# Optimization experiments

Hardware: AMD Instinct MI355X
Metric: run time of the kernel (lower is better)

## Reference

```python
import jax, jax.numpy as jnp
import numpy as np

B, N, E = 32, 196, 512      # batch, image regions, encoder_dim
D, EMB, V = 512, 512, 32000  # decoder_dim, embedding_dim, vocab
MAXLEN = 65


def setup_inputs() -> dict:
    key = jax.random.key(0)
    ks = jax.random.split(key, 16)
    s = lambda *sh: 1.0 / np.sqrt(sh[-1])
    return {
        "image_features": jax.random.normal(ks[0], (B, N, E), jnp.float32),
        "captions": jax.random.randint(ks[1], (B, MAXLEN), 0, V),
        "emb": jax.random.normal(ks[2], (V, EMB), jnp.float32) * 0.02,
        "Wh0": jax.random.normal(ks[3], (D, E), jnp.float32) * s(E),
        "bh0": jnp.zeros((D,), jnp.float32),
        "Wc0": jax.random.normal(ks[4], (D, E), jnp.float32) * s(E),
        "bc0": jnp.zeros((D,), jnp.float32),
        "Wenc": jax.random.normal(ks[5], (D, E), jnp.float32) * s(E),
        "Wdec": jax.random.normal(ks[6], (D, D), jnp.float32) * s(D),
        "v_att": jax.random.normal(ks[7], (D,), jnp.float32) * s(D),
        "W_ih": jax.random.normal(ks[8], (4 * D, EMB + E), jnp.float32) * s(EMB + E),
        "b_ih": jnp.zeros((4 * D,), jnp.float32),
        "W_hh": jax.random.normal(ks[9], (4 * D, D), jnp.float32) * s(D),
        "b_hh": jnp.zeros((4 * D,), jnp.float32),
        "Wfc": jax.random.normal(ks[10], (V, D), jnp.float32) * s(D),
        "bfc": jnp.zeros((V,), jnp.float32),
    }


def reference(image_features, captions, emb, Wh0, bh0, Wc0, bc0,
              Wenc, Wdec, v_att, W_ih, b_ih, W_hh, b_hh, Wfc, bfc):
    seq_len = captions.shape[1] - 1
    emb_caps = emb[captions]                     # [B, maxlen, EMB]
    xs = jnp.swapaxes(emb_caps[:, :seq_len], 0, 1)  # [T, B, EMB]

    feat_mean = image_features.mean(axis=1)      # [B, E]
    h0 = feat_mean @ Wh0.T + bh0                 # [B, D]
    c0 = feat_mean @ Wc0.T + bc0
    feat_proj = jnp.einsum('bne,de->bnd', image_features, Wenc)  # [B, N, D]

    def step(carry, xt):
        h, c = carry
        # Bahdanau additive attention over the N image regions
        e = jnp.einsum('bnd,d->bn', jnp.tanh(feat_proj + (h @ Wdec.T)[:, None, :]), v_att)
        alpha = jax.nn.softmax(e, axis=-1)                       # [B, N]
        ctx = jnp.einsum('bn,bne->be', alpha, image_features)    # [B, E]
        x = jnp.concatenate([xt, ctx], axis=-1)                  # [B, EMB+E]
        gates = x @ W_ih.T + b_ih + h @ W_hh.T + b_hh            # [B, 4D]
        i, f, g, o = jnp.split(gates, 4, axis=-1)
        c_new = jax.nn.sigmoid(f) * c + jax.nn.sigmoid(i) * jnp.tanh(g)
        h_new = jax.nn.sigmoid(o) * jnp.tanh(c_new)
        out = h_new @ Wfc.T + bfc                                # [B, V]
        return (h_new, c_new), (out, alpha)
    # dropout_p=0.0 -> dropout is identity (eval-mode reference)
    _, (outs, alphas) = jax.lax.scan(step, (h0, c0), xs)
    outputs = jnp.swapaxes(outs, 0, 1)            # [B, T, V]
    attention_weights = jnp.swapaxes(alphas, 0, 1)  # [B, T, N]
    return outputs, attention_weights
```

## Files before the change

kernel.cpp:

```cpp
#include <hip/hip_runtime.h>
#include <cstdint>
#include <cstddef>

typedef _Float16 half2_t __attribute__((ext_vector_type(2)));
typedef _Float16 half4_t __attribute__((ext_vector_type(4)));
typedef _Float16 half8_t __attribute__((ext_vector_type(8)));
typedef float    float4_t __attribute__((ext_vector_type(4)));

#define CAPLEN 65
#define PTLD 200
#define BARSTRIDE 32

#define AT_LD(p)     __hip_atomic_load((p), __ATOMIC_RELAXED, __HIP_MEMORY_SCOPE_AGENT)
#define AT_ST(p, v)  __hip_atomic_store((p), (v), __ATOMIC_RELAXED, __HIP_MEMORY_SCOPE_AGENT)

#if defined(__has_builtin)
#if __has_builtin(__builtin_amdgcn_fdot2)
#define HAS_FDOT2 1
#endif
#endif

__device__ __forceinline__ float fdot2f(half2_t a, half2_t b, float c) {
#ifdef HAS_FDOT2
  return __builtin_amdgcn_fdot2(a, b, c, false);
#else
  return c + (float)a[0]*(float)b[0] + (float)a[1]*(float)b[1];
#endif
}

__device__ __forceinline__ float fast_tanh(float x) {
  float e = __expf(2.f*x);
  return 1.f - 2.f/(e + 1.f);
}
__device__ __forceinline__ float fast_sig(float x) {
  return 1.f/(1.f + __expf(-x));
}

__global__ void cvt_k(const float* __restrict__ s, _Float16* __restrict__ d, int n) {
  int i = (blockIdx.x*blockDim.x + threadIdx.x)*4;
  if (i < n) {
    float4 v = *(const float4*)(s + i);
    half4_t h;
    h[0] = (_Float16)v.x; h[1] = (_Float16)v.y; h[2] = (_Float16)v.z; h[3] = (_Float16)v.w;
    *(half4_t*)(d + i) = h;
  }
}

__global__ void bias_sum_k(const float* __restrict__ a, const float* __restrict__ b,
                           float* __restrict__ o, unsigned* __restrict__ bar) {
  int i = blockIdx.x*blockDim.x + threadIdx.x;
  if (i < 2048) o[i] = a[i] + b[i];
  for (int j = i; j < 32*8*BARSTRIDE; j += 2048) bar[j] = 0u;
}

__global__ void gather_emb_k(const float* __restrict__ emb, const int* __restrict__ cap,
                             _Float16* __restrict__ X) {
  int r = blockIdx.x;
  int t = r >> 5, b = r & 31;
  int tok = cap[b*CAPLEN + t];
  const float* s = emb + (size_t)tok*512;
  _Float16* d = X + (size_t)r*512;
  for (int k = threadIdx.x; k < 512; k += blockDim.x) d[k] = (_Float16)s[k];
}

__global__ void init_state_k(const float* __restrict__ imgf,
                             const float* __restrict__ Wh0, const float* __restrict__ bh0,
                             const float* __restrict__ Wc0, const float* __restrict__ bc0,
                             float* __restrict__ c_state, unsigned* __restrict__ hpub2) {
  __shared__ float fm[512];
  __shared__ float hsh[512];
  int b = blockIdx.x, tid = threadIdx.x;
  for (int dI = tid; dI < 512; dI += 256) {
    float s = 0.f;
    const float* p = imgf + ((size_t)b*196)*512 + dI;
    for (int n = 0; n < 196; n++) s += p[(size_t)n*512];
    fm[dI] = s * (1.f/196.f);
  }
  __syncthreads();
  for (int dI = tid; dI < 512; dI += 256) {
    const float* wh = Wh0 + (size_t)dI*512;
    const float* wc = Wc0 + (size_t)dI*512;
    float h = bh0[dI], c = bc0[dI];
    for (int k = 0; k < 512; k++) { h += fm[k]*wh[k]; c += fm[k]*wc[k]; }
    hsh[dI] = h;
    c_state[b*512 + dI] = c;
  }
  __syncthreads();
  {
    half2_t h2; h2[0] = (_Float16)hsh[2*tid]; h2[1] = (_Float16)hsh[2*tid+1];
    union { half2_t h; unsigned u; } cv; cv.h = h2;
    hpub2[b*256 + tid] = cv.u;
  }
}

template<int MODE>
__global__ void __launch_bounds__(256) gemm_abt_k(const _Float16* __restrict__ A, int lda,
    const _Float16* __restrict__ B, int ldb, void* __restrict__ Cp, int ldc,
    const float* __restrict__ bias, int K) {
  int wave = threadIdx.x >> 6, lane = threadIdx.x & 63;
  int m0 = blockIdx.y*128 + (wave >> 1)*64;
  int n0 = blockIdx.x*128 + (wave & 1)*64;
  int lr = lane & 15, quad = lane >> 4;
  float4_t acc[4][4];
  #pragma unroll
  for (int i = 0; i < 4; i++)
    #pragma unroll
    for (int j = 0; j < 4; j++)
      acc[i][j] = (float4_t){0.f, 0.f, 0.f, 0.f};
  const _Float16* Ap = A + (size_t)(m0 + lr)*lda + quad*8;
  const _Float16* Bp = B + (size_t)(n0 + lr)*ldb + quad*8;
  for (int k0 = 0; k0 < K; k0 += 32) {
    half8_t af[4], bf[4];
    #pragma unroll
    for (int i = 0; i < 4; i++) af[i] = *(const half8_t*)(Ap + (size_t)i*16*lda + k0);
    #pragma unroll
    for (int i = 0; i < 4; i++) bf[i] = *(const half8_t*)(Bp + (size_t)i*16*ldb + k0);
    #pragma unroll
    for (int mi = 0; mi < 4; mi++)
      #pragma unroll
      for (int ni = 0; ni < 4; ni++)
        acc[mi][ni] = __builtin_amdgcn_mfma_f32_16x16x32_f16(af[mi], bf[ni], acc[mi][ni], 0, 0, 0);
  }
  #pragma unroll
  for (int mi = 0; mi < 4; mi++) {
    #pragma unroll
    for (int ni = 0; ni < 4; ni++) {
      int col = n0 + ni*16 + lr;
      float bv = (MODE == 1) ? 0.f : bias[col];
      #pragma unroll
      for (int r = 0; r < 4; r++) {
        int row = m0 + mi*16 + quad*4 + r;
        if (MODE == 1) {
          ((_Float16*)Cp)[(size_t)row*ldc + col] = (_Float16)acc[mi][ni][r];
        } else {
          ((float*)Cp)[(size_t)row*ldc + col] = acc[mi][ni][r] + bv;
        }
      }
    }
  }
}

__global__ void __launch_bounds__(256) gemm_pt_k(const _Float16* __restrict__ A, int lda,
    const _Float16* __restrict__ Bimg, _Float16* __restrict__ Cpt, int mrows) {
  int z = blockIdx.z;
  const _Float16* B = Bimg + (size_t)z*196*512;
  _Float16* C = Cpt + (size_t)z*mrows*PTLD;
  int wave = threadIdx.x >> 6, lane = threadIdx.x & 63;
  int m0 = blockIdx.y*128 + (wave >> 1)*64;
  int n0 = blockIdx.x*128 + (wave & 1)*64;
  int lr = lane & 15, quad = lane >> 4;
  float4_t acc[4][4];
  #pragma unroll
  for (int i = 0; i < 4; i++)
    #pragma unroll
    for (int j = 0; j < 4; j++)
      acc[i][j] = (float4_t){0.f, 0.f, 0.f, 0.f};
  const _Float16* Ap = A + (size_t)(m0 + lr)*lda + quad*8;
  const _Float16* Bp = B + (size_t)(n0 + lr)*512 + quad*8;
  for (int k0 = 0; k0 < 512; k0 += 32) {
    half8_t af[4], bf[4];
    #pragma unroll
    for (int i = 0; i < 4; i++) af[i] = *(const half8_t*)(Ap + (size_t)i*16*lda + k0);
    #pragma unroll
    for (int i = 0; i < 4; i++) bf[i] = *(const half8_t*)(Bp + (size_t)i*16*512 + k0);
    #pragma unroll
    for (int mi = 0; mi < 4; mi++)
      #pragma unroll
      for (int ni = 0; ni < 4; ni++)
        acc[mi][ni] = __builtin_amdgcn_mfma_f32_16x16x32_f16(af[mi], bf[ni], acc[mi][ni], 0, 0, 0);
  }
  #pragma unroll
  for (int mi = 0; mi < 4; mi++) {
    #pragma unroll
    for (int ni = 0; ni < 4; ni++) {
      int col = n0 + ni*16 + lr;
      if (col < PTLD) {
        #pragma unroll
        for (int r = 0; r < 4; r++) {
          int row = m0 + mi*16 + quad*4 + r;
          C[(size_t)row*PTLD + col] = (_Float16)acc[mi][ni][r];
        }
      }
    }
  }
}

__device__ __forceinline__ void sbar_arrive(unsigned* __restrict__ slots, int r,
                                            unsigned target, int tid) {
  __syncthreads();
  if (tid == 0) AT_ST(slots + r*BARSTRIDE, target);
}
__device__ __forceinline__ void sbar_wait(unsigned* __restrict__ slots,
                                          unsigned target, int tid) {
  if (tid < 8) {
    while (AT_LD(slots + tid*BARSTRIDE) < target) __builtin_amdgcn_s_sleep(1);
  }
  __syncthreads();
}

__global__ void __launch_bounds__(512) loop_k(
    const _Float16* __restrict__ Wdec_h,
    const _Float16* __restrict__ Whh_h,
    const _Float16* __restrict__ fproj_T,
    const _Float16* __restrict__ P_T,
    const float*    __restrict__ Xg,
    const float*    __restrict__ v_att,
    const float*    __restrict__ c_init,
    unsigned*       __restrict__ hpub2,
    float*          __restrict__ epub,
    _Float16*       __restrict__ H_h,
    float*          __restrict__ out_alpha,
    unsigned*       __restrict__ bar) {
  __shared__ _Float16 P_lds[98*256*2];
  __shared__ _Float16 fp_lds[64*PTLD];
  __shared__ __align__(16) unsigned hl_u[256];
  __shared__ _Float16 Hbuf[64*64];
  __shared__ float abuf[25*64];
  __shared__ float vlf[64];
  __shared__ float hwf[64];
  __shared__ float ep[2][256];
  __shared__ float redA[8];
  __shared__ float redB[8];
  __shared__ float sa[256];
  __shared__ float sm2[512];
  __shared__ float hnl[64];
  int bid = blockIdx.x, tid = threadIdx.x;
  int r = bid & 7, b = bid >> 3;
  unsigned* slots = bar + b*8*BARSTRIDE;
  int row = tid & 255, half = tid >> 8;
  int typ = row >> 6, dl = row & 63;
  int grow = typ*512 + r*64 + dl;
  int lane = tid & 63;

  if (tid < 64) vlf[tid] = v_att[r*64 + tid];
  float c_reg = (tid < 64) ? c_init[b*512 + r*64 + tid] : 0.f;

  if (tid < 256) {
    const _Float16* pp = P_T + ((size_t)b*2048 + grow)*PTLD;
    half2_t* P2 = (half2_t*)P_lds;
    for (int k8 = 0; k8 < 24; k8++) {
      half8_t v8 = *(const half8_t*)(pp + k8*8);
      #pragma unroll
      for (int j2 = 0; j2 < 4; j2++) {
        half2_t h2; h2[0] = v8[2*j2]; h2[1] = v8[2*j2+1];
        P2[(k8*4 + j2)*256 + row] = h2;
      }
    }
    half4_t v4 = *(const half4_t*)(pp + 192);
    half2_t a2; a2[0] = v4[0]; a2[1] = v4[1];
    half2_t b2; b2[0] = v4[2]; b2[1] = v4[3];
    P2[96*256 + row] = a2;
    P2[97*256 + row] = b2;
  } else {
    for (int i = tid - 256; i < 64*25; i += 256) {
      int d = i/25, c = i - d*25;
      *(half8_t*)(fp_lds + d*PTLD + c*8) =
        *(const half8_t*)(fproj_T + ((size_t)(b*512 + r*64 + d))*PTLD + c*8);
    }
  }
  int eBase = (r < 4) ? r*25 : 100 + (r-4)*24;
  int eCnt  = (r < 4) ? 25 : 24;

  for (int t = 0; t < 64; ++t) {
    if (tid < 256) hl_u[tid] = AT_LD(hpub2 + b*256 + tid);
    float xg = (half == 1) ? Xg[((size_t)t*32 + b)*2048 + grow] : 0.f;
    __syncthreads();
    {
      int dim = tid >> 3, s = tid & 7;
      const half8_t* wr = (const half8_t*)(Wdec_h + (size_t)(r*64 + dim)*512 + s*64);
      const half8_t* hh = ((const half8_t*)(const _Float16*)hl_u) + s*8;
      float a = 0.f;
      #pragma unroll
      for (int k8 = 0; k8 < 8; k8++) {
        half8_t w8 = wr[k8]; half8_t h8 = hh[k8];
        const half2_t* wp = (const half2_t*)&w8;
        const half2_t* hp = (const half2_t*)&h8;
        a = fdot2f(wp[0], hp[0], a);
        a = fdot2f(wp[1], hp[1], a);
        a = fdot2f(wp[2], hp[2], a);
        a = fdot2f(wp[3], hp[3], a);
      }
      a += __shfl_xor(a, 1);
      a += __shfl_xor(a, 2);
      a += __shfl_xor(a, 4);
      if (s == 0) hwf[dim] = a;
    }
    __syncthreads();
    {
      float a = 0.f;
      if (row < 196) {
        #pragma unroll 8
        for (int j = 0; j < 32; j++) {
          int dd = half*32 + j;
          a += vlf[dd] * fast_tanh((float)fp_lds[dd*PTLD + row] + hwf[dd]);
        }
      }
      ep[half][row] = a;
    }
    __syncthreads();
    if (tid < 196) AT_ST(epub + ((size_t)b*8 + r)*256 + tid, ep[0][tid] + ep[1][tid]);
    sbar_arrive(slots, r, 2*(unsigned)t + 1, tid);
    float gacc = xg;
    {
      const half8_t* wr = (const half8_t*)(Whh_h + (size_t)grow*512 + half*256);
      const half8_t* hh = ((const half8_t*)(const _Float16*)hl_u) + half*32;
      for (int k8 = 0; k8 < 32; k8++) {
        half8_t w8 = wr[k8]; half8_t h8 = hh[k8];
        const half2_t* wp = (const half2_t*)&w8;
        const half2_t* hp = (const half2_t*)&h8;
        gacc = fdot2f(wp[0], hp[0], gacc);
        gacc = fdot2f(wp[1], hp[1], gacc);
        gacc = fdot2f(wp[2], hp[2], gacc);
        gacc = fdot2f(wp[3], hp[3], gacc);
      }
    }
    sbar_wait(slots, 2*(unsigned)t + 1, tid);

    float ee = -1e30f;
    if (tid < 196) {
      float s0 = 0.f;
      #pragma unroll
      for (int rr = 0; rr < 8; rr++)
        s0 += AT_LD(epub + ((size_t)b*8 + rr)*256 + tid);
      ee = s0;
    }
    {
      float m = ee;
      #pragma unroll
      for (int off = 32; off > 0; off >>= 1) m = fmaxf(m, __shfl_xor(m, off));
      if (lane == 0) redA[tid >> 6] = m;
    }
    __syncthreads();
    float mx = redA[0];
    #pragma unroll
    for (int i = 1; i < 8; i++) mx = fmaxf(mx, redA[i]);
    float ex = (tid < 196) ? __expf(ee - mx) : 0.f;
    {
      float s = ex;
      #pragma unroll
      for (int off = 32; off > 0; off >>= 1) s += __shfl_xor(s, off);
      if (lane == 0) redB[tid >> 6] = s;
    }
    __syncthreads();
    float tot = redB[0];
    #pragma unroll
    for (int i = 1; i < 8; i++) tot += redB[i];
    float al = ex * (1.f/tot);
    if (tid < 256) sa[tid] = al;
    if (tid >= eBase && tid < eBase + eCnt)
      abuf[(tid - eBase)*64 + t] = al;
    __syncthreads();
    {
      const half2_t* P2 = (const half2_t*)P_lds;
      const float2*  sap = (const float2*)sa;
      int n2b = half*49;
      #pragma unroll 7
      for (int n2 = n2b; n2 < n2b + 49; n2++) {
        half2_t p = P2[n2*256 + row];
        float2 s2 = sap[n2];
        gacc += s2.x*(float)p[0] + s2.y*(float)p[1];
      }
      sm2[tid] = gacc;
    }
    __syncthreads();
    if (tid < 64) {
      float ig = sm2[tid]       + sm2[tid + 256];
      float fg = sm2[64 + tid]  + sm2[tid + 320];
      float gg = sm2[128 + tid] + sm2[tid + 384];
      float og = sm2[192 + tid] + sm2[tid + 448];
      float cn = fast_sig(fg)*c_reg + fast_sig(ig)*fast_tanh(gg);
      float hn = fast_sig(og)*fast_tanh(cn);
      c_reg = cn;
      hnl[tid] = hn;
      Hbuf[t*64 + tid] = (_Float16)hn;
    }
    __syncthreads();
    if (tid < 32) {
      half2_t h2; h2[0] = (_Float16)hnl[2*tid]; h2[1] = (_Float16)hnl[2*tid+1];
      union { half2_t h; unsigned u; } cv; cv.h = h2;
      AT_ST(hpub2 + b*256 + r*32 + tid, cv.u);
    }
    sbar_arrive(slots, r, 2*(unsigned)t + 2, tid);
    sbar_wait(slots, 2*(unsigned)t + 2, tid);
  }

  for (int i = tid; i < 64*64; i += 512) {
    int t = i >> 6, d = i & 63;
    H_h[((size_t)t*32 + b)*512 + r*64 + d] = Hbuf[i];
  }
  for (int i = tid; i < eCnt*64; i += 512) {
    int ln = i >> 6, t = i & 63;
    out_alpha[((size_t)b*64 + t)*196 + eBase + ln] = abuf[ln*64 + t];
  }
}

__global__ void __launch_bounds__(512) logits_k(const _Float16* __restrict__ A,
    const _Float16* __restrict__ Bw, float* __restrict__ C,
    const float* __restrict__ bias) {
  int wave = threadIdx.x >> 6, lane = threadIdx.x & 63;
  int lr = lane & 15, quad = lane >> 4;
  int waveM = wave >> 1, waveN = wave & 1;
  int n0 = blockIdx.x*128 + waveN*64;
  const _Float16* Bp = Bw + (size_t)(n0 + lr)*512 + quad*8;
  float bv[4];
  #pragma unroll
  for (int ni = 0; ni < 4; ni++) bv[ni] = bias[n0 + ni*16 + lr];
  for (int it = 0; it < 4; ++it) {
    int m0 = (blockIdx.y*16 + it*4 + waveM)*64;
    const _Float16* Ap = A + (size_t)(m0 + lr)*512 + quad*8;
    float4_t acc[4][4];
    #pragma unroll
    for (int i = 0; i < 4; i++)
      #pragma unroll
      for (int j = 0; j < 4; j++)
        acc[i][j] = (float4_t){0.f, 0.f, 0.f, 0.f};
    for (int k0 = 0; k0 < 512; k0 += 32) {
      half8_t af[4], bf[4];
      #pragma unroll
      for (int i = 0; i < 4; i++) af[i] = *(const half8_t*)(Ap + (size_t)i*16*512 + k0);
      #pragma unroll
      for (int i = 0; i < 4; i++) bf[i] = *(const half8_t*)(Bp + (size_t)i*16*512 + k0);
      #pragma unroll
      for (int mi = 0; mi < 4; mi++)
        #pragma unroll
        for (int ni = 0; ni < 4; ni++)
          acc[mi][ni] = __builtin_amdgcn_mfma_f32_16x16x32_f16(af[mi], bf[ni], acc[mi][ni], 0, 0, 0);
    }
    #pragma unroll
    for (int mi = 0; mi < 4; mi++) {
      #pragma unroll
      for (int ni = 0; ni < 4; ni++) {
        int col = n0 + ni*16 + lr;
        #pragma unroll
        for (int r = 0; r < 4; r++) {
          int row = m0 + mi*16 + quad*4 + r;
          size_t orow = (size_t)((row & 31)*64 + (row >> 5));
          __builtin_nontemporal_store(acc[mi][ni][r] + bv[ni], C + orow*32000 + col);
        }
      }
    }
  }
}

extern "C" void kernel_launch(void* const* d_in, const int* in_sizes, int n_in,
                              void* d_out, int out_size, void* d_ws, size_t ws_size,
                              hipStream_t stream) {
  const float* imgf  = (const float*)d_in[0];
  const int*   cap   = (const int*)d_in[1];
  const float* emb   = (const float*)d_in[2];
  const float* Wh0   = (const float*)d_in[3];
  const float* bh0   = (const float*)d_in[4];
  const float* Wc0   = (const float*)d_in[5];
  const float* bc0   = (const float*)d_in[6];
  const float* Wenc  = (const float*)d_in[7];
  const float* Wdec  = (const float*)d_in[8];
  const float* v_att = (const float*)d_in[9];
  const float* W_ih  = (const float*)d_in[10];
  const float* b_ih  = (const float*)d_in[11];
  const float* W_hh  = (const float*)d_in[12];
  const float* b_hh  = (const float*)d_in[13];
  const float* Wfc   = (const float*)d_in[14];
  const float* bfc   = (const float*)d_in[15];
  float* out = (float*)d_out;
  (void)in_sizes; (void)n_in; (void)out_size; (void)ws_size;

  char* ws = (char*)d_ws;
  size_t off = 0;
  auto alloc = [&](size_t bytes) -> void* {
    void* p = ws + off;
    off += (bytes + 255) & ~(size_t)255;
    return p;
  };
  _Float16* Wenc_h  = (_Float16*)alloc((size_t)512*512*2);
  _Float16* Wdec_h  = (_Float16*)alloc((size_t)512*512*2);
  _Float16* Wih_h   = (_Float16*)alloc((size_t)2048*1024*2);
  _Float16* Whh_h   = (_Float16*)alloc((size_t)2048*512*2);
  _Float16* Wfc_h   = (_Float16*)alloc((size_t)32000*512*2);
  _Float16* imgf_h  = (_Float16*)alloc((size_t)32*196*512*2);
  _Float16* fproj_T = (_Float16*)alloc((size_t)32*512*PTLD*2);
  _Float16* P_T     = (_Float16*)alloc((size_t)32*2048*PTLD*2);
  _Float16* X_h     = (_Float16*)alloc((size_t)64*32*512*2);
  float*    Xg      = (float*)alloc((size_t)64*32*2048*4);
  float*    bsum    = (float*)alloc((size_t)2048*4);
  float*    c_state = (float*)alloc((size_t)32*512*4);
  unsigned* hpub2   = (unsigned*)alloc((size_t)32*256*4);
  float*    epub    = (float*)alloc((size_t)32*8*256*4);
  _Float16* H_h     = (_Float16*)alloc((size_t)2048*512*2);
  unsigned* bar     = (unsigned*)alloc((size_t)32*8*BARSTRIDE*4);

  auto cvt = [&](const float* s, _Float16* d, int n) {
    cvt_k<<<dim3((n/4 + 255)/256), dim3(256), 0, stream>>>(s, d, n);
  };
  cvt(Wenc, Wenc_h, 512*512);
  cvt(Wdec, Wdec_h, 512*512);
  cvt(W_ih, Wih_h, 2048*1024);
  cvt(W_hh, Whh_h, 2048*512);
  cvt(Wfc,  Wfc_h, 32000*512);
  cvt(imgf, imgf_h, 32*196*512);
  bias_sum_k<<<dim3(8), dim3(256), 0, stream>>>(b_ih, b_hh, bsum, bar);
  gather_emb_k<<<dim3(2048), dim3(256), 0, stream>>>(emb, cap, X_h);
  init_state_k<<<dim3(32), dim3(256), 0, stream>>>(imgf, Wh0, bh0, Wc0, bc0, c_state, hpub2);
  gemm_pt_k<<<dim3(2, 4, 32), dim3(256), 0, stream>>>(Wenc_h, 512, imgf_h, fproj_T, 512);
  gemm_pt_k<<<dim3(2, 16, 32), dim3(256), 0, stream>>>(Wih_h + 512, 1024, imgf_h, P_T, 2048);
  gemm_abt_k<0><<<dim3(16, 16), dim3(256), 0, stream>>>(X_h, 512, Wih_h, 1024, Xg, 2048, bsum, 512);

  float* out_alpha = out + (size_t)32*64*32000;
  loop_k<<<dim3(256), dim3(512), 0, stream>>>(Wdec_h, Whh_h, fproj_T, P_T, Xg,
      v_att, c_state, hpub2, epub, H_h, out_alpha, bar);
  logits_k<<<dim3(250, 2), dim3(512), 0, stream>>>(H_h, Wfc_h, out, bfc);
}
```

Measured before the change: 2.027 ms.

## Split recurrent loop kernel across 16 smaller blocks per batch row

The persistent LSTM/attention loop kernel now uses 512 blocks of 256 threads instead of 256 blocks of 512. Each block owns 32 hidden dims instead of 64, so per-block LDS and per-step work shrink and two blocks can sit on each CU. The attention-energy partials are stored transposed so each region's 16 partials are contiguous, and the cross-block barrier is widened to 16 slots. The risk is more blocks to synchronise each step, plus reliance on all 512 blocks being resident at once for the spin barrier.

```diff
diff --git a/kernel.cpp b/kernel.cpp
--- a/kernel.cpp
+++ b/kernel.cpp
@@ -10,6 +10,7 @@
 #define CAPLEN 65
 #define PTLD 200
 #define BARSTRIDE 32
+#define CTLWORDS (32*16*BARSTRIDE)
 
 #define AT_LD(p)     __hip_atomic_load((p), __ATOMIC_RELAXED, __HIP_MEMORY_SCOPE_AGENT)
 #define AT_ST(p, v)  __hip_atomic_store((p), (v), __ATOMIC_RELAXED, __HIP_MEMORY_SCOPE_AGENT)
@@ -50,7 +51,7 @@
                            float* __restrict__ o, unsigned* __restrict__ bar) {
   int i = blockIdx.x*blockDim.x + threadIdx.x;
   if (i < 2048) o[i] = a[i] + b[i];
-  for (int j = i; j < 32*8*BARSTRIDE; j += 2048) bar[j] = 0u;
+  for (int j = i; j < CTLWORDS; j += 2048) bar[j] = 0u;
 }
 
 __global__ void gather_emb_k(const float* __restrict__ emb, const int* __restrict__ cap,
@@ -192,13 +193,13 @@
 }
 __device__ __forceinline__ void sbar_wait(unsigned* __restrict__ slots,
                                           unsigned target, int tid) {
-  if (tid < 8) {
+  if (tid < 16) {
     while (AT_LD(slots + tid*BARSTRIDE) < target) __builtin_amdgcn_s_sleep(1);
   }
   __syncthreads();
 }
 
-__global__ void __launch_bounds__(512) loop_k(
+__global__ void __launch_bounds__(256, 2) loop_k(
     const _Float16* __restrict__ Wdec_h,
     const _Float16* __restrict__ Whh_h,
     const _Float16* __restrict__ fproj_T,
@@ -211,63 +212,63 @@
     _Float16*       __restrict__ H_h,
     float*          __restrict__ out_alpha,
     unsigned*       __restrict__ bar) {
-  __shared__ _Float16 P_lds[98*256*2];
-  __shared__ _Float16 fp_lds[64*PTLD];
+  __shared__ _Float16 P_lds[98*128*2];
+  __shared__ _Float16 fp_lds[32*PTLD];
   __shared__ __align__(16) unsigned hl_u[256];
-  __shared__ _Float16 Hbuf[64*64];
-  __shared__ float abuf[25*64];
-  __shared__ float vlf[64];
-  __shared__ float hwf[64];
-  __shared__ float ep[2][256];
-  __shared__ float redA[8];
-  __shared__ float redB[8];
+  __shared__ _Float16 Hbuf[64*32];
+  __shared__ float abuf[13*64];
+  __shared__ float vlf[32];
+  __shared__ float hwf[32];
+  __shared__ float redA[4];
+  __shared__ float redB[4];
   __shared__ float sa[256];
-  __shared__ float sm2[512];
-  __shared__ float hnl[64];
+  __shared__ float sm2[256];
+  __shared__ float hnl[32];
   int bid = blockIdx.x, tid = threadIdx.x;
-  int r = bid & 7, b = bid >> 3;
-  unsigned* slots = bar + b*8*BARSTRIDE;
-  int row = tid & 255, half = tid >> 8;
-  int typ = row >> 6, dl = row & 63;
-  int grow = typ*512 + r*64 + dl;
+  int r = bid & 15, b = bid >> 4;
+  unsigned* slots = bar + b*16*BARSTRIDE;
+  int rowLoc = tid >> 1, nhalf = tid & 1;
+  int typ = rowLoc >> 5, dl = rowLoc & 31;
+  int grow = typ*512 + r*32 + dl;
   int lane = tid & 63;
 
-  if (tid < 64) vlf[tid] = v_att[r*64 + tid];
-  float c_reg = (tid < 64) ? c_init[b*512 + r*64 + tid] : 0.f;
-
-  if (tid < 256) {
-    const _Float16* pp = P_T + ((size_t)b*2048 + grow)*PTLD;
+  if (tid < 32) vlf[tid] = v_att[r*32 + tid];
+  float c_reg = (tid < 32) ? c_init[b*512 + r*32 + tid] : 0.f;
+
+  if (tid < 128) {
+    int rl = tid;
+    int pg = (rl >> 5)*512 + r*32 + (rl & 31);
+    const _Float16* pp = P_T + ((size_t)b*2048 + pg)*PTLD;
     half2_t* P2 = (half2_t*)P_lds;
     for (int k8 = 0; k8 < 24; k8++) {
       half8_t v8 = *(const half8_t*)(pp + k8*8);
       #pragma unroll
       for (int j2 = 0; j2 < 4; j2++) {
         half2_t h2; h2[0] = v8[2*j2]; h2[1] = v8[2*j2+1];
-        P2[(k8*4 + j2)*256 + row] = h2;
+        P2[(k8*4 + j2)*128 + rl] = h2;
       }
     }
     half4_t v4 = *(const half4_t*)(pp + 192);
     half2_t a2; a2[0] = v4[0]; a2[1] = v4[1];
     half2_t b2; b2[0] = v4[2]; b2[1] = v4[3];
-    P2[96*256 + row] = a2;
-    P2[97*256 + row] = b2;
-  } else {
-    for (int i = tid - 256; i < 64*25; i += 256) {
-      int d = i/25, c = i - d*25;
-      *(half8_t*)(fp_lds + d*PTLD + c*8) =
-        *(const half8_t*)(fproj_T + ((size_t)(b*512 + r*64 + d))*PTLD + c*8);
-    }
-  }
-  int eBase = (r < 4) ? r*25 : 100 + (r-4)*24;
-  int eCnt  = (r < 4) ? 25 : 24;
+    P2[96*128 + rl] = a2;
+    P2[97*128 + rl] = b2;
+  }
+  for (int i = tid; i < 32*25; i += 256) {
+    int d = i/25, c = i - d*25;
+    *(half8_t*)(fp_lds + d*PTLD + c*8) =
+      *(const half8_t*)(fproj_T + ((size_t)(b*512 + r*32 + d))*PTLD + c*8);
+  }
+  int eBase = (r < 4) ? r*13 : 52 + (r-4)*12;
+  int eCnt  = (r < 4) ? 13 : 12;
 
   for (int t = 0; t < 64; ++t) {
-    if (tid < 256) hl_u[tid] = AT_LD(hpub2 + b*256 + tid);
-    float xg = (half == 1) ? Xg[((size_t)t*32 + b)*2048 + grow] : 0.f;
+    hl_u[tid] = AT_LD(hpub2 + b*256 + tid);
+    float xg = (nhalf == 0) ? Xg[((size_t)t*32 + b)*2048 + grow] : 0.f;
     __syncthreads();
     {
       int dim = tid >> 3, s = tid & 7;
-      const half8_t* wr = (const half8_t*)(Wdec_h + (size_t)(r*64 + dim)*512 + s*64);
+      const half8_t* wr = (const half8_t*)(Wdec_h + (size_t)(r*32 + dim)*512 + s*64);
       const half8_t* hh = ((const half8_t*)(const _Float16*)hl_u) + s*8;
       float a = 0.f;
       #pragma unroll
@@ -286,24 +287,18 @@
       if (s == 0) hwf[dim] = a;
     }
     __syncthreads();
-    {
+    if (tid < 196) {
       float a = 0.f;
-      if (row < 196) {
-        #pragma unroll 8
-        for (int j = 0; j < 32; j++) {
-          int dd = half*32 + j;
-          a += vlf[dd] * fast_tanh((float)fp_lds[dd*PTLD + row] + hwf[dd]);
-        }
-      }
-      ep[half][row] = a;
-    }
-    __syncthreads();
-    if (tid < 196) AT_ST(epub + ((size_t)b*8 + r)*256 + tid, ep[0][tid] + ep[1][tid]);
+      #pragma unroll 8
+      for (int dd = 0; dd < 32; dd++)
+        a += vlf[dd] * fast_tanh((float)fp_lds[dd*PTLD + tid] + hwf[dd]);
+      AT_ST(epub + ((size_t)b*196 + tid)*16 + r, a);
+    }
     sbar_arrive(slots, r, 2*(unsigned)t + 1, tid);
     float gacc = xg;
     {
-      const half8_t* wr = (const half8_t*)(Whh_h + (size_t)grow*512 + half*256);
-      const half8_t* hh = ((const half8_t*)(const _Float16*)hl_u) + half*32;
+      const half8_t* wr = (const half8_t*)(Whh_h + (size_t)grow*512 + nhalf*256);
+      const half8_t* hh = ((const half8_t*)(const _Float16*)hl_u) + nhalf*32;
       for (int k8 = 0; k8 < 32; k8++) {
         half8_t w8 = wr[k8]; half8_t h8 = hh[k8];
         const half2_t* wp = (const half2_t*)&w8;
@@ -318,10 +313,10 @@
 
     float ee = -1e30f;
     if (tid < 196) {
+      const float* pb = epub + ((size_t)b*196 + tid)*16;
       float s0 = 0.f;
       #pragma unroll
-      for (int rr = 0; rr < 8; rr++)
-        s0 += AT_LD(epub + ((size_t)b*8 + rr)*256 + tid);
+      for (int rr = 0; rr < 16; rr++) s0 += AT_LD(pb + rr);
       ee = s0;
     }
     {
@@ -331,9 +326,7 @@
       if (lane == 0) redA[tid >> 6] = m;
     }
     __syncthreads();
-    float mx = redA[0];
-    #pragma unroll
-    for (int i = 1; i < 8; i++) mx = fmaxf(mx, redA[i]);
+    float mx = fmaxf(fmaxf(redA[0], redA[1]), fmaxf(redA[2], redA[3]));
     float ex = (tid < 196) ? __expf(ee - mx) : 0.f;
     {
       float s = ex;
@@ -342,55 +335,53 @@
       if (lane == 0) redB[tid >> 6] = s;
     }
     __syncthreads();
-    float tot = redB[0];
-    #pragma unroll
-    for (int i = 1; i < 8; i++) tot += redB[i];
+    float tot = (redB[0] + redB[1]) + (redB[2] + redB[3]);
     float al = ex * (1.f/tot);
-    if (tid < 256) sa[tid] = al;
+    sa[tid] = al;
     if (tid >= eBase && tid < eBase + eCnt)
       abuf[(tid - eBase)*64 + t] = al;
     __syncthreads();
     {
       const half2_t* P2 = (const half2_t*)P_lds;
       const float2*  sap = (const float2*)sa;
-      int n2b = half*49;
+      int n2b = nhalf*49;
       #pragma unroll 7
       for (int n2 = n2b; n2 < n2b + 49; n2++) {
-        half2_t p = P2[n2*256 + row];
+        half2_t p = P2[n2*128 + rowLoc];
         float2 s2 = sap[n2];
         gacc += s2.x*(float)p[0] + s2.y*(float)p[1];
       }
       sm2[tid] = gacc;
     }
     __syncthreads();
-    if (tid < 64) {
-      float ig = sm2[tid]       + sm2[tid + 256];
-      float fg = sm2[64 + tid]  + sm2[tid + 320];
-      float gg = sm2[128 + tid] + sm2[tid + 384];
-      float og = sm2[192 + tid] + sm2[tid + 448];
+    if (tid < 32) {
+      float ig = sm2[2*tid]            + sm2[2*tid + 1];
+      float fg = sm2[2*(32 + tid)]     + sm2[2*(32 + tid) + 1];
+      float gg = sm2[2*(64 + tid)]     + sm2[2*(64 + tid) + 1];
+      float og = sm2[2*(96 + tid)]     + sm2[2*(96 + tid) + 1];
       float cn = fast_sig(fg)*c_reg + fast_sig(ig)*fast_tanh(gg);
       float hn = fast_sig(og)*fast_tanh(cn);
       c_reg = cn;
       hnl[tid] = hn;
-      Hbuf[t*64 + tid] = (_Float16)hn;
-    }
-    __syncthreads();
-    if (tid < 32) {
+      Hbuf[t*32 + tid] = (_Float16)hn;
+    }
+    __syncthreads();
+    if (tid < 16) {
       half2_t h2; h2[0] = (_Float16)hnl[2*tid]; h2[1] = (_Float16)hnl[2*tid+1];
       union { half2_t h; unsigned u; } cv; cv.h = h2;
-      AT_ST(hpub2 + b*256 + r*32 + tid, cv.u);
+      AT_ST(hpub2 + b*256 + r*16 + tid, cv.u);
     }
     sbar_arrive(slots, r, 2*(unsigned)t + 2, tid);
     sbar_wait(slots, 2*(unsigned)t + 2, tid);
   }
 
-  for (int i = tid; i < 64*64; i += 512) {
-    int t = i >> 6, d = i & 63;
-    H_h[((size_t)t*32 + b)*512 + r*64 + d] = Hbuf[i];
-  }
-  for (int i = tid; i < eCnt*64; i += 512) {
-    int ln = i >> 6, t = i & 63;
-    out_alpha[((size_t)b*64 + t)*196 + eBase + ln] = abuf[ln*64 + t];
+  for (int i = tid; i < 64*32; i += 256) {
+    int t = i >> 5, d = i & 31;
+    H_h[((size_t)t*32 + b)*512 + r*32 + d] = Hbuf[i];
+  }
+  for (int i = tid; i < eCnt*64; i += 256) {
+    int ln = i >> 6, tt = i & 63;
+    out_alpha[((size_t)b*64 + tt)*196 + eBase + ln] = abuf[ln*64 + tt];
   }
 }
 
@@ -484,9 +475,9 @@
   float*    bsum    = (float*)alloc((size_t)2048*4);
   float*    c_state = (float*)alloc((size_t)32*512*4);
   unsigned* hpub2   = (unsigned*)alloc((size_t)32*256*4);
-  float*    epub    = (float*)alloc((size_t)32*8*256*4);
+  float*    epub    = (float*)alloc((size_t)32*196*16*4);
   _Float16* H_h     = (_Float16*)alloc((size_t)2048*512*2);
-  unsigned* bar     = (unsigned*)alloc((size_t)32*8*BARSTRIDE*4);
+  unsigned* bar     = (unsigned*)alloc((size_t)CTLWORDS*4);
 
   auto cvt = [&](const float* s, _Float16* d, int n) {
     cvt_k<<<dim3((n/4 + 255)/256), dim3(256), 0, stream>>>(s, d, n);
@@ -505,7 +496,7 @@
   gemm_abt_k<0><<<dim3(16, 16), dim3(256), 0, stream>>>(X_h, 512, Wih_h, 1024, Xg, 2048, bsum, 512);
 
   float* out_alpha = out + (size_t)32*64*32000;
-  loop_k<<<dim3(256), dim3(512), 0, stream>>>(Wdec_h, Whh_h, fproj_T, P_T, Xg,
+  loop_k<<<dim3(512), dim3(256), 0, stream>>>(Wdec_h, Whh_h, fproj_T, P_T, Xg,
       v_att, c_state, hpub2, epub, H_h, out_alpha, bar);
   logits_k<<<dim3(250, 2), dim3(512), 0, stream>>>(H_h, Wfc_h, out, bfc);
 }
```

After: 2.129 ms. 5.0% more time.

## Replace per-step group barriers with step-tagged double-buffered data flags

Applied to the files above, without the earlier changes.

The separate counter barriers between the 8 blocks of each batch are removed. Each published value (the h half-pairs and the partial attention energies) now goes out as a 64-bit word carrying the step index in its upper half, in double-buffered slots, and consumers spin until the tag matches. This collapses barrier arrive/wait plus data load into a single polled load, removing two global round trips per step. The cost is twice the memory traffic per published value and per-element polling, and correctness now depends on 64-bit atomic visibility and on the initial tag fill.

```diff
diff --git a/kernel.cpp b/kernel.cpp
--- a/kernel.cpp
+++ b/kernel.cpp
@@ -9,7 +9,6 @@
 
 #define CAPLEN 65
 #define PTLD 200
-#define BARSTRIDE 32
 
 #define AT_LD(p)     __hip_atomic_load((p), __ATOMIC_RELAXED, __HIP_MEMORY_SCOPE_AGENT)
 #define AT_ST(p, v)  __hip_atomic_store((p), (v), __ATOMIC_RELAXED, __HIP_MEMORY_SCOPE_AGENT)
@@ -46,11 +45,18 @@
   }
 }
 
+__global__ void fill_tags_k(unsigned long long* __restrict__ h64,
+                            unsigned long long* __restrict__ e64) {
+  int stride = gridDim.x*blockDim.x;
+  int i = blockIdx.x*blockDim.x + threadIdx.x;
+  for (int j = i; j < 2*32*256; j += stride) h64[j] = ~0ull;
+  for (int j = i; j < 2*32*256*8; j += stride) e64[j] = ~0ull;
+}
+
 __global__ void bias_sum_k(const float* __restrict__ a, const float* __restrict__ b,
-                           float* __restrict__ o, unsigned* __restrict__ bar) {
+                           float* __restrict__ o) {
   int i = blockIdx.x*blockDim.x + threadIdx.x;
   if (i < 2048) o[i] = a[i] + b[i];
-  for (int j = i; j < 32*8*BARSTRIDE; j += 2048) bar[j] = 0u;
 }
 
 __global__ void gather_emb_k(const float* __restrict__ emb, const int* __restrict__ cap,
@@ -66,7 +72,8 @@
 __global__ void init_state_k(const float* __restrict__ imgf,
                              const float* __restrict__ Wh0, const float* __restrict__ bh0,
                              const float* __restrict__ Wc0, const float* __restrict__ bc0,
-                             float* __restrict__ c_state, unsigned* __restrict__ hpub2) {
+                             float* __restrict__ c_state,
+                             unsigned long long* __restrict__ hpub64) {
   __shared__ float fm[512];
   __shared__ float hsh[512];
   int b = blockIdx.x, tid = threadIdx.x;
@@ -89,7 +96,7 @@
   {
     half2_t h2; h2[0] = (_Float16)hsh[2*tid]; h2[1] = (_Float16)hsh[2*tid+1];
     union { half2_t h; unsigned u; } cv; cv.h = h2;
-    hpub2[b*256 + tid] = cv.u;
+    hpub64[(size_t)b*256 + tid] = (unsigned long long)cv.u;
   }
 }
 
@@ -185,19 +192,6 @@
   }
 }
 
-__device__ __forceinline__ void sbar_arrive(unsigned* __restrict__ slots, int r,
-                                            unsigned target, int tid) {
-  __syncthreads();
-  if (tid == 0) AT_ST(slots + r*BARSTRIDE, target);
-}
-__device__ __forceinline__ void sbar_wait(unsigned* __restrict__ slots,
-                                          unsigned target, int tid) {
-  if (tid < 8) {
-    while (AT_LD(slots + tid*BARSTRIDE) < target) __builtin_amdgcn_s_sleep(1);
-  }
-  __syncthreads();
-}
-
 __global__ void __launch_bounds__(512) loop_k(
     const _Float16* __restrict__ Wdec_h,
     const _Float16* __restrict__ Whh_h,
@@ -206,11 +200,11 @@
     const float*    __restrict__ Xg,
     const float*    __restrict__ v_att,
     const float*    __restrict__ c_init,
-    unsigned*       __restrict__ hpub2,
-    float*          __restrict__ epub,
+    unsigned long long* __restrict__ hpub64,
+    unsigned long long* __restrict__ epub64,
     _Float16*       __restrict__ H_h,
-    float*          __restrict__ out_alpha,
-    unsigned*       __restrict__ bar) {
+    float*          __restrict__ out_alpha)
+{
   __shared__ _Float16 P_lds[98*256*2];
   __shared__ _Float16 fp_lds[64*PTLD];
   __shared__ __align__(16) unsigned hl_u[256];
@@ -226,7 +220,6 @@
   __shared__ float hnl[64];
   int bid = blockIdx.x, tid = threadIdx.x;
   int r = bid & 7, b = bid >> 3;
-  unsigned* slots = bar + b*8*BARSTRIDE;
   int row = tid & 255, half = tid >> 8;
   int typ = row >> 6, dl = row & 63;
   int grow = typ*512 + r*64 + dl;
@@ -262,7 +255,15 @@
   int eCnt  = (r < 4) ? 25 : 24;
 
   for (int t = 0; t < 64; ++t) {
-    if (tid < 256) hl_u[tid] = AT_LD(hpub2 + b*256 + tid);
+    if (tid < 256) {
+      const unsigned long long* hp = hpub64 + ((size_t)(t & 1)*32 + b)*256 + tid;
+      unsigned long long v = AT_LD(hp);
+      while ((unsigned)(v >> 32) != (unsigned)t) {
+        __builtin_amdgcn_s_sleep(1);
+        v = AT_LD(hp);
+      }
+      hl_u[tid] = (unsigned)v;
+    }
     float xg = (half == 1) ? Xg[((size_t)t*32 + b)*2048 + grow] : 0.f;
     __syncthreads();
     {
@@ -298,8 +299,11 @@
       ep[half][row] = a;
     }
     __syncthreads();
-    if (tid < 196) AT_ST(epub + ((size_t)b*8 + r)*256 + tid, ep[0][tid] + ep[1][tid]);
-    sbar_arrive(slots, r, 2*(unsigned)t + 1, tid);
+    if (tid < 196) {
+      union { float f; unsigned u; } c; c.f = ep[0][tid] + ep[1][tid];
+      AT_ST(epub64 + (((size_t)(t & 1)*32 + b)*256 + tid)*8 + r,
+            ((unsigned long long)(unsigned)t << 32) | (unsigned long long)c.u);
+    }
     float gacc = xg;
     {
       const half8_t* wr = (const half8_t*)(Whh_h + (size_t)grow*512 + half*256);
@@ -314,15 +318,25 @@
         gacc = fdot2f(wp[3], hp[3], gacc);
       }
     }
-    sbar_wait(slots, 2*(unsigned)t + 1, tid);
-
     float ee = -1e30f;
     if (tid < 196) {
-      float s0 = 0.f;
-      #pragma unroll
-      for (int rr = 0; rr < 8; rr++)
-        s0 += AT_LD(epub + ((size_t)b*8 + rr)*256 + tid);
-      ee = s0;
+      const unsigned long long* pb = epub64 + (((size_t)(t & 1)*32 + b)*256 + tid)*8;
+      float vals[8];
+      unsigned done = 0;
+      while (done != 0xFFu) {
+        #pragma unroll
+        for (int rr = 0; rr < 8; rr++) {
+          if (!(done & (1u << rr))) {
+            unsigned long long v = AT_LD(pb + rr);
+            if ((unsigned)(v >> 32) == (unsigned)t) {
+              union { unsigned u; float f; } c; c.u = (unsigned)v;
+              vals[rr] = c.f; done |= (1u << rr);
+            }
+          }
+        }
+        if (done != 0xFFu) __builtin_amdgcn_s_sleep(1);
+      }
+      ee = ((vals[0]+vals[1]) + (vals[2]+vals[3])) + ((vals[4]+vals[5]) + (vals[6]+vals[7]));
     }
     {
       float m = ee;
@@ -378,10 +392,10 @@
     if (tid < 32) {
       half2_t h2; h2[0] = (_Float16)hnl[2*tid]; h2[1] = (_Float16)hnl[2*tid+1];
       union { half2_t h; unsigned u; } cv; cv.h = h2;
-      AT_ST(hpub2 + b*256 + r*32 + tid, cv.u);
-    }
-    sbar_arrive(slots, r, 2*(unsigned)t + 2, tid);
-    sbar_wait(slots, 2*(unsigned)t + 2, tid);
+      AT_ST(hpub64 + ((size_t)((t + 1) & 1)*32 + b)*256 + r*32 + tid,
+            ((unsigned long long)(unsigned)(t + 1) << 32) | (unsigned long long)cv.u);
+    }
+    __syncthreads();
   }
 
   for (int i = tid; i < 64*64; i += 512) {
@@ -389,8 +403,8 @@
     H_h[((size_t)t*32 + b)*512 + r*64 + d] = Hbuf[i];
   }
   for (int i = tid; i < eCnt*64; i += 512) {
-    int ln = i >> 6, t = i & 63;
-    out_alpha[((size_t)b*64 + t)*196 + eBase + ln] = abuf[ln*64 + t];
+    int ln = i >> 6, tt = i & 63;
+    out_alpha[((size_t)b*64 + tt)*196 + eBase + ln] = abuf[ln*64 + tt];
   }
 }
 
@@ -483,10 +497,11 @@
   float*    Xg      = (float*)alloc((size_t)64*32*2048*4);
   float*    bsum    = (float*)alloc((size_t)2048*4);
   float*    c_state = (float*)alloc((size_t)32*512*4);
-  unsigned* hpub2   = (unsigned*)alloc((size_t)32*256*4);
-  float*    epub    = (float*)alloc((size_t)32*8*256*4);
+  unsigned long long* hpub64 = (unsigned long long*)alloc((size_t)2*32*256*8);
+  unsigned long long* epub64 = (unsigned long long*)alloc((size_t)2*32*256*8*8);
   _Float16* H_h     = (_Float16*)alloc((size_t)2048*512*2);
-  unsigned* bar     = (unsigned*)alloc((size_t)32*8*BARSTRIDE*4);
+
+  fill_tags_k<<<dim3(256), dim3(256), 0, stream>>>(hpub64, epub64);
 
   auto cvt = [&](const float* s, _Float16* d, int n) {
     cvt_k<<<dim3((n/4 + 255)/256), dim3(256), 0, stream>>>(s, d, n);
@@ -497,15 +512,15 @@
   cvt(W_hh, Whh_h, 2048*512);
   cvt(Wfc,  Wfc_h, 32000*512);
   cvt(imgf, imgf_h, 32*196*512);
-  bias_sum_k<<<dim3(8), dim3(256), 0, stream>>>(b_ih, b_hh, bsum, bar);
+  bias_sum_k<<<dim3(8), dim3(256), 0, stream>>>(b_ih, b_hh, bsum);
   gather_emb_k<<<dim3(2048), dim3(256), 0, stream>>>(emb, cap, X_h);
-  init_state_k<<<dim3(32), dim3(256), 0, stream>>>(imgf, Wh0, bh0, Wc0, bc0, c_state, hpub2);
+  init_state_k<<<dim3(32), dim3(256), 0, stream>>>(imgf, Wh0, bh0, Wc0, bc0, c_state, hpub64);
   gemm_pt_k<<<dim3(2, 4, 32), dim3(256), 0, stream>>>(Wenc_h, 512, imgf_h, fproj_T, 512);
   gemm_pt_k<<<dim3(2, 16, 32), dim3(256), 0, stream>>>(Wih_h + 512, 1024, imgf_h, P_T, 2048);
   gemm_abt_k<0><<<dim3(16, 16), dim3(256), 0, stream>>>(X_h, 512, Wih_h, 1024, Xg, 2048, bsum, 512);
 
   float* out_alpha = out + (size_t)32*64*32000;
   loop_k<<<dim3(256), dim3(512), 0, stream>>>(Wdec_h, Whh_h, fproj_T, P_T, Xg,
-      v_att, c_state, hpub2, epub, H_h, out_alpha, bar);
+      v_att, c_state, hpub64, epub64, H_h, out_alpha);
   logits_k<<<dim3(250, 2), dim3(512), 0, stream>>>(H_h, Wfc_h, out, bfc);
 }
```

After: 1.970 ms. -2.8%, faster.
